# Kernel optimization log

Hardware: AMD Instinct MI355X
Metric: run time of the kernel (lower is better)

## Reference

```python
import jax, jax.numpy as jnp
import numpy as np

LOC_SIZE, CID_SIZE, UID_SIZE, TIM_SIZE = 10000, 300, 1000, 48
LOC_EMB, CID_EMB, UID_EMB, TIM_EMB = 256, 64, 64, 32
HID, ENC_HID = 500, 250            # hidden_size, history_hidden_size
SEQ, TGT = 2048, 256
INPUT = LOC_EMB + TIM_EMB + CID_EMB  # 352


def setup_inputs() -> dict:
    key = jax.random.key(0)
    ks = jax.random.split(key, 32)
    n = lambda i, shape, s=0.05: (jax.random.normal(ks[i], shape, dtype=jnp.float32) * s)
    d = {}
    d["loc"] = jax.random.randint(ks[0], (SEQ, 1), 0, LOC_SIZE)
    d["tim"] = jax.random.randint(ks[1], (SEQ, 1), 0, TIM_SIZE)
    d["cid"] = jax.random.randint(ks[2], (SEQ, 1), 0, CID_SIZE)
    d["uid"] = jax.random.randint(ks[3], (1,), 0, UID_SIZE)
    d["target"] = jax.random.randint(ks[4], (TGT, 1), 0, LOC_SIZE)
    d["target_len"] = TGT
    d["time_sim_matrix"] = jax.random.uniform(ks[5], (TIM_SIZE, TIM_SIZE), dtype=jnp.float32)
    # keep distances away from 0 since the model computes 1/dist
    d["poi_distance_matrix"] = jax.random.uniform(ks[6], (LOC_SIZE, LOC_SIZE), dtype=jnp.float32, minval=0.1, maxval=2.0)
    d["poi_cid_tim"] = jax.random.uniform(ks[7], (TIM_SIZE, CID_SIZE), dtype=jnp.float32)
    # embedding tables (emb_loc/emb_cid are pretrained+frozen in the original)
    d["weight"] = n(8, (LOC_SIZE, LOC_EMB))
    d["weight_cid"] = n(9, (CID_SIZE, CID_EMB))
    d["emb_uid_w"] = n(10, (UID_SIZE, UID_EMB))
    d["emb_tim_w"] = n(11, (TIM_SIZE, TIM_EMB))
    # bidirectional encoder LSTM (hidden 250), gate order i,f,g,o like torch
    d["enc_Wih_f"] = n(12, (4 * ENC_HID, INPUT))
    d["enc_Whh_f"] = n(13, (4 * ENC_HID, ENC_HID))
    d["enc_b_f"] = jnp.zeros((4 * ENC_HID,), jnp.float32)
    d["enc_Wih_b"] = n(14, (4 * ENC_HID, INPUT))
    d["enc_Whh_b"] = n(15, (4 * ENC_HID, ENC_HID))
    d["enc_b_b"] = jnp.zeros((4 * ENC_HID,), jnp.float32)
    # decoder LSTM (hidden 500)
    d["dec_Wih"] = n(16, (4 * HID, INPUT))
    d["dec_Whh"] = n(17, (4 * HID, HID))
    d["dec_b"] = jnp.zeros((4 * HID,), jnp.float32)
    # linear layers
    d["fc_user_w"] = n(18, (HID, UID_EMB))
    d["fc_user_b"] = jnp.zeros((HID,), jnp.float32)
    d["fc_final_w"] = n(19, (LOC_SIZE, 3 * HID))
    d["fc_final_b"] = jnp.zeros((LOC_SIZE,), jnp.float32)
    d["fc_final2_w"] = n(20, (HID, 3 * HID))
    d["fc_final2_b"] = jnp.zeros((HID,), jnp.float32)
    return d


def _lstm(x, Wih, Whh, b, H):
    """Single-layer LSTM, batch=1. x: [T, D] -> hs: [T, H]."""
    h0 = jnp.zeros((H,), x.dtype)
    c0 = jnp.zeros((H,), x.dtype)

    def step(carry, xt):
        h, c = carry
        z = Wih @ xt + Whh @ h + b
        i, f, g, o = jnp.split(z, 4)
        c = jax.nn.sigmoid(f) * c + jax.nn.sigmoid(i) * jnp.tanh(g)
        h = jax.nn.sigmoid(o) * jnp.tanh(c)
        return (h, c), h

    _, hs = jax.lax.scan(step, (h0, c0), x)
    return hs


def _table_attn(history, current, table, invert=False, causal=False):
    """Vectorized replacement for the nested-loop lookup attention.
    energies[i, j] = table[current[i], history[j]] (or its reciprocal),
    upper triangle left at 0 for the self-attn variants (as in the original),
    then softmax over the full row (torch F.softmax default dim=1 on 2D)."""
    e = table[current[:, None], history[None, :]]
    if invert:
        e = 1.0 / e
    if causal:
        nn_ = e.shape[0]
        e = jnp.where(jnp.tril(jnp.ones((nn_, nn_), bool)), e, jnp.zeros((), e.dtype))
    return jax.nn.softmax(e, axis=-1)


def reference(loc, tim, cid, uid, target, target_len,
              time_sim_matrix, poi_distance_matrix, poi_cid_tim,
              weight, weight_cid, emb_uid_w, emb_tim_w,
              enc_Wih_f, enc_Whh_f, enc_b_f, enc_Wih_b, enc_Whh_b, enc_b_b,
              dec_Wih, dec_Whh, dec_b,
              fc_user_w, fc_user_b, fc_final_w, fc_final_b, fc_final2_w, fc_final2_b):
    T = int(target_len)
    loc_f, tim_f, cid_f = loc[:, 0], tim[:, 0], cid[:, 0]

    # cross attention: current window attends to history via lookup tables
    attn_cid_time = _table_attn(cid_f[:-T], tim_f[-T:], poi_cid_tim)
    attn_loc = _table_attn(loc_f[:-T], loc_f[-T:], poi_distance_matrix, invert=True)
    attn_time = _table_attn(tim_f[:-T], tim_f[-T:], time_sim_matrix)
    # self attention on the current window (lower-triangular fill)
    self_cid_time = _table_attn(cid_f[-T:], tim_f[-T:], poi_cid_tim, causal=True)
    self_loc = _table_attn(loc_f[-T:], loc_f[-T:], poi_distance_matrix, invert=True, causal=True)
    self_time = _table_attn(tim_f[-T:], tim_f[-T:], time_sim_matrix, causal=True)

    # embeddings (dropout is identity in eval)
    x = jnp.concatenate([weight[loc_f], emb_tim_w[tim_f], weight_cid[cid_f]], axis=1)  # [SEQ, INPUT]
    hist_x, tgt_x = x[:-T], x[-T:]

    # bidirectional encoder over history
    hf = _lstm(hist_x, enc_Wih_f, enc_Whh_f, enc_b_f, ENC_HID)
    hb = _lstm(hist_x[::-1], enc_Wih_b, enc_Whh_b, enc_b_b, ENC_HID)[::-1]
    hidden_history = jnp.concatenate([hf, hb], axis=1)  # [SEQ-T, 2*ENC_HID=500]

    # decoder over current window
    hidden_state = _lstm(tgt_x, dec_Wih, dec_Whh, dec_b, HID)  # [T, 500]

    target_emb = weight[target[:, 0]]  # [T, LOC_EMB]

    uid_emb = emb_uid_w[uid] @ fc_user_w.T + fc_user_b  # [1, 500]
    user_attn = jax.nn.softmax(uid_emb @ hidden_history.T, axis=-1)  # [1, hist]
    context_user = user_attn @ hidden_history  # [1, 500]

    context = (attn_loc + attn_time + attn_cid_time) @ hidden_history  # [T, 500]
    hidden_state = (self_loc + self_time + self_cid_time) @ hidden_state  # [T, 500]

    hidden_state_all = hidden_state + uid_emb  # broadcast of repeat
    out = jnp.concatenate([hidden_state_all, context,
                           jnp.broadcast_to(context_user, (T, HID))], axis=1)  # [T, 1500]
    y = out @ fc_final_w.T + fc_final_b    # [T, LOC_SIZE]
    y1 = out @ fc_final2_w.T + fc_final2_b  # [T, HID]
    score = jax.nn.log_softmax(y, axis=-1)
    return score, y1, target_emb
```

## Files before the change

### kernel.cpp

```cpp
#include <hip/hip_runtime.h>
#include <stdint.h>

#define HIST 1792
#define TGT 256
#define SEQ 2048
#define INPUT 352
#define EHID 250
#define HID 500

typedef _Float16 h2_t __attribute__((ext_vector_type(2)));

static __device__ __forceinline__ float fdot2(uint32_t a, uint32_t b, float c) {
  return __builtin_amdgcn_fdot2(__builtin_bit_cast(h2_t, a),
                                __builtin_bit_cast(h2_t, b), c, false);
}
static __device__ __forceinline__ uint32_t packh2(float lo, float hi) {
  h2_t h; h[0] = (_Float16)lo; h[1] = (_Float16)hi;
  return __builtin_bit_cast(uint32_t, h);
}
static __device__ __forceinline__ uint4 packq(const float* p) {
  uint4 r;
  r.x = packh2(p[0], p[1]); r.y = packh2(p[2], p[3]);
  r.z = packh2(p[4], p[5]); r.w = packh2(p[6], p[7]);
  return r;
}
static __device__ __forceinline__ float dotq(uint4 w, uint4 h, float acc) {
  acc = fdot2(w.x, h.x, acc); acc = fdot2(w.y, h.y, acc);
  acc = fdot2(w.z, h.z, acc); acc = fdot2(w.w, h.w, acc);
  return acc;
}
static __device__ __forceinline__ float sigf(float x) {
  x = fminf(fmaxf(x, -30.f), 30.f);
  return 1.f / (1.f + __expf(-x));
}
static __device__ __forceinline__ float tanh_f(float x) {
  x = fminf(fmaxf(x, -15.f), 15.f);
  float e = __expf(2.f * x);
  return (e - 1.f) / (e + 1.f);
}
static __device__ __forceinline__ void spin_flag(volatile int* f) {
  while (__hip_atomic_load(f, __ATOMIC_ACQUIRE, __HIP_MEMORY_SCOPE_AGENT) == 0)
    __builtin_amdgcn_s_sleep(2);
}
#define AW(dst, src) asm("v_accvgpr_write_b32 %0, %1" : "=a"(dst) : "v"(src))
#define AR(dst, src) asm("v_accvgpr_read_b32 %0, %1" : "=v"(dst) : "a"(src))
#define ARQ(dst, arr, base) do { AR(dst.x, arr[(base)+0]); AR(dst.y, arr[(base)+1]); AR(dst.z, arr[(base)+2]); AR(dst.w, arr[(base)+3]); } while(0)

__global__ void k_embed(const int* __restrict__ loc, const int* __restrict__ tim,
                        const int* __restrict__ cid, const int* __restrict__ target,
                        const float* __restrict__ weight, const float* __restrict__ emb_tim_w,
                        const float* __restrict__ weight_cid,
                        float* __restrict__ x, float* __restrict__ te) {
  int t = blockIdx.x, tid = threadIdx.x;
  if (t < SEQ) {
    int l = loc[t], tm = tim[t], cd = cid[t];
    float* xr = x + (size_t)t * INPUT;
    for (int k = tid; k < 256; k += blockDim.x) xr[k] = weight[(size_t)l * 256 + k];
    for (int k = tid; k < 32; k += blockDim.x)  xr[256 + k] = emb_tim_w[tm * 32 + k];
    for (int k = tid; k < 64; k += blockDim.x)  xr[288 + k] = weight_cid[cd * 64 + k];
  } else {
    int i = t - SEQ;
    int tg = target[i];
    for (int k = tid; k < 256; k += blockDim.x) te[(size_t)i * 256 + k] = weight[(size_t)tg * 256 + k];
  }
}

__global__ void k_gemm_t16(const float* __restrict__ A, int lda,
                           const float* __restrict__ W, const float* __restrict__ bias,
                           float* __restrict__ C, int ldc,
                           int M, int N, int K, int revA) {
  __shared__ uint32_t AsP[8][65];
  __shared__ uint32_t WsP[8][65];
  const int bn = blockIdx.x * 64, bm = blockIdx.y * 64;
  const int tid = threadIdx.x;
  const int tx = tid & 15, ty = tid >> 4;
  float acc[4][4] = {};
  for (int k0 = 0; k0 < K; k0 += 16) {
    for (int i = tid; i < 512; i += 256) {
      int m = i & 63, kk = i >> 6;
      int gm = bm + m, gk = k0 + 2 * kk;
      float v0 = 0.f, v1 = 0.f;
      if (gm < M) {
        int am = revA ? (M - 1 - gm) : gm;
        if (gk < K)     v0 = A[(size_t)am * lda + gk];
        if (gk + 1 < K) v1 = A[(size_t)am * lda + gk + 1];
      }
      AsP[kk][m] = packh2(v0, v1);
    }
    for (int i = tid; i < 512; i += 256) {
      int n = i & 63, kk = i >> 6;
      int gn = bn + n, gk = k0 + 2 * kk;
      float v0 = 0.f, v1 = 0.f;
      if (gn < N) {
        if (gk < K)     v0 = W[(size_t)gn * K + gk];
        if (gk + 1 < K) v1 = W[(size_t)gn * K + gk + 1];
      }
      WsP[kk][n] = packh2(v0, v1);
    }
    __syncthreads();
#pragma unroll
    for (int kk = 0; kk < 8; kk++) {
      uint32_t a0 = AsP[kk][ty * 4 + 0], a1 = AsP[kk][ty * 4 + 1], a2 = AsP[kk][ty * 4 + 2], a3 = AsP[kk][ty * 4 + 3];
      uint32_t b0 = WsP[kk][tx * 4 + 0], b1 = WsP[kk][tx * 4 + 1], b2 = WsP[kk][tx * 4 + 2], b3 = WsP[kk][tx * 4 + 3];
      acc[0][0] = fdot2(a0, b0, acc[0][0]); acc[0][1] = fdot2(a0, b1, acc[0][1]);
      acc[0][2] = fdot2(a0, b2, acc[0][2]); acc[0][3] = fdot2(a0, b3, acc[0][3]);
      acc[1][0] = fdot2(a1, b0, acc[1][0]); acc[1][1] = fdot2(a1, b1, acc[1][1]);
      acc[1][2] = fdot2(a1, b2, acc[1][2]); acc[1][3] = fdot2(a1, b3, acc[1][3]);
      acc[2][0] = fdot2(a2, b0, acc[2][0]); acc[2][1] = fdot2(a2, b1, acc[2][1]);
      acc[2][2] = fdot2(a2, b2, acc[2][2]); acc[2][3] = fdot2(a2, b3, acc[2][3]);
      acc[3][0] = fdot2(a3, b0, acc[3][0]); acc[3][1] = fdot2(a3, b1, acc[3][1]);
      acc[3][2] = fdot2(a3, b2, acc[3][2]); acc[3][3] = fdot2(a3, b3, acc[3][3]);
    }
    __syncthreads();
  }
  for (int i = 0; i < 4; i++) {
    int gm = bm + ty * 4 + i; if (gm >= M) continue;
    for (int j = 0; j < 4; j++) {
      int gn = bn + tx * 4 + j; if (gn >= N) continue;
      C[(size_t)gm * ldc + gn] = acc[i][j] + (bias ? bias[gn] : 0.f);
    }
  }
}

__global__ void k_gemm_nn16(const float* __restrict__ A, int lda,
                            const float* __restrict__ B, int ldb,
                            const float* __restrict__ addvec,
                            float* __restrict__ C, int ldc,
                            int M, int N, int K) {
  __shared__ uint32_t AsP[8][65];
  __shared__ uint32_t BsP[8][65];
  const int bn = blockIdx.x * 64, bm = blockIdx.y * 64;
  const int tid = threadIdx.x;
  const int tx = tid & 15, ty = tid >> 4;
  float acc[4][4] = {};
  for (int k0 = 0; k0 < K; k0 += 16) {
    for (int i = tid; i < 512; i += 256) {
      int m = i & 63, kk = i >> 6;
      int gm = bm + m, gk = k0 + 2 * kk;
      float v0 = 0.f, v1 = 0.f;
      if (gm < M) {
        if (gk < K)     v0 = A[(size_t)gm * lda + gk];
        if (gk + 1 < K) v1 = A[(size_t)gm * lda + gk + 1];
      }
      AsP[kk][m] = packh2(v0, v1);
    }
    for (int i = tid; i < 512; i += 256) {
      int n = i & 63, kk = i >> 6;
      int gn = bn + n, gk = k0 + 2 * kk;
      float v0 = 0.f, v1 = 0.f;
      if (gn < N) {
        if (gk < K)     v0 = B[(size_t)gk * ldb + gn];
        if (gk + 1 < K) v1 = B[(size_t)(gk + 1) * ldb + gn];
      }
      BsP[kk][n] = packh2(v0, v1);
    }
    __syncthreads();
#pragma unroll
    for (int kk = 0; kk < 8; kk++) {
      uint32_t a0 = AsP[kk][ty * 4 + 0], a1 = AsP[kk][ty * 4 + 1], a2 = AsP[kk][ty * 4 + 2], a3 = AsP[kk][ty * 4 + 3];
      uint32_t b0 = BsP[kk][tx * 4 + 0], b1 = BsP[kk][tx * 4 + 1], b2 = BsP[kk][tx * 4 + 2], b3 = BsP[kk][tx * 4 + 3];
      acc[0][0] = fdot2(a0, b0, acc[0][0]); acc[0][1] = fdot2(a0, b1, acc[0][1]);
      acc[0][2] = fdot2(a0, b2, acc[0][2]); acc[0][3] = fdot2(a0, b3, acc[0][3]);
      acc[1][0] = fdot2(a1, b0, acc[1][0]); acc[1][1] = fdot2(a1, b1, acc[1][1]);
      acc[1][2] = fdot2(a1, b2, acc[1][2]); acc[1][3] = fdot2(a1, b3, acc[1][3]);
      acc[2][0] = fdot2(a2, b0, acc[2][0]); acc[2][1] = fdot2(a2, b1, acc[2][1]);
      acc[2][2] = fdot2(a2, b2, acc[2][2]); acc[2][3] = fdot2(a2, b3, acc[2][3]);
      acc[3][0] = fdot2(a3, b0, acc[3][0]); acc[3][1] = fdot2(a3, b1, acc[3][1]);
      acc[3][2] = fdot2(a3, b2, acc[3][2]); acc[3][3] = fdot2(a3, b3, acc[3][3]);
    }
    __syncthreads();
  }
  for (int i = 0; i < 4; i++) {
    int gm = bm + ty * 4 + i; if (gm >= M) continue;
    for (int j = 0; j < 4; j++) {
      int gn = bn + tx * 4 + j; if (gn >= N) continue;
      C[(size_t)gm * ldc + gn] = acc[i][j] + (addvec ? addvec[gn] : 0.f);
    }
  }
}

#define WQL 12
#define WBYTES (WQL * 512 * 16)
__launch_bounds__(512)
__global__ void k_lstm(const float* __restrict__ A_f, const float* __restrict__ A_b,
                       const float* __restrict__ A_d,
                       const float* __restrict__ Whh_f, const float* __restrict__ Whh_b,
                       const float* __restrict__ Whh_d,
                       float* __restrict__ hh, float* __restrict__ hdec,
                       float* zpub, uint32_t* hpub, int* flag_z, int* flag_h) {
  const int b = blockIdx.x;
  const int tid = threadIdx.x;
  __shared__ __align__(16) unsigned char smem[WBYTES + 2048];
  uint4* wl = (uint4*)smem;
  uint4* hbuf = (uint4*)(smem + WBYTES);

  if (tid < 128) hbuf[tid] = make_uint4(0, 0, 0, 0);

  if (b < 2) {
    const float* A = (b == 0) ? A_f : A_b;
    const float* Whh = (b == 0) ? Whh_f : Whh_b;
    const bool act = tid < 500;
    const int cell = act ? (tid >> 1) : 249;
    const int role = tid & 1;
    const int row0 = role * 250 + cell;
    const int row1 = 500 + role * 250 + cell;
    uint4 wv0[10], wv1[10];
    uint32_t wa[128];
    if (act) {
      const float* wr0 = Whh + (size_t)row0 * EHID;
      const float* wr1 = Whh + (size_t)row1 * EHID;
#pragma unroll
      for (int q = 0; q < 6; q++) {
        float t0[8], t1[8];
#pragma unroll
        for (int cc = 0; cc < 8; cc++) {
          int col = 208 + 8 * q + cc;
          t0[cc] = (col < EHID) ? wr0[col] : 0.f;
          t1[cc] = (col < EHID) ? wr1[col] : 0.f;
        }
        wl[(q * 2 + 0) * 512 + tid] = packq(t0);
        wl[(q * 2 + 1) * 512 + tid] = packq(t1);
      }
#pragma unroll
      for (int k = 0; k < 16; k++) {
        uint4 p0 = packq(wr0 + 8 * (10 + k));
        uint4 p1 = packq(wr1 + 8 * (10 + k));
        AW(wa[k * 4 + 0], p0.x); AW(wa[k * 4 + 1], p0.y);
        AW(wa[k * 4 + 2], p0.z); AW(wa[k * 4 + 3], p0.w);
        AW(wa[64 + k * 4 + 0], p1.x); AW(wa[64 + k * 4 + 1], p1.y);
        AW(wa[64 + k * 4 + 2], p1.z); AW(wa[64 + k * 4 + 3], p1.w);
      }
#pragma unroll
      for (int q = 0; q < 10; q++) { wv0[q] = packq(wr0 + 8 * q); wv1[q] = packq(wr1 + 8 * q); }
    }
    float c = 0.f;
    float aA = act ? A[row0] : 0.f;
    float aB = act ? A[row1] : 0.f;
    __syncthreads();
    for (int t = 0; t < HIST; t++) {
      const uint4* hb = hbuf + (t & 1) * 32;
      float z_r0 = 0.f, z_r1 = 0.f;
      if (act) {
        float z0 = aA, z1 = aB, y0 = 0.f, y1 = 0.f;
        int tn = (t + 1 < HIST) ? t + 1 : t;
        aA = A[tn * 1000 + row0];
        aB = A[tn * 1000 + row1];
#pragma unroll
        for (int q = 0; q < 10; q++) {
          uint4 hq = hb[q];
          z0 = dotq(wv0[q], hq, z0);
          z1 = dotq(wv1[q], hq, z1);
        }
#pragma unroll
        for (int k = 0; k < 16; k++) {
          uint4 hq = hb[10 + k];
          uint4 u0, u1;
          ARQ(u0, wa, k * 4);
          ARQ(u1, wa, 64 + k * 4);
          y0 = dotq(u0, hq, y0);
          y1 = dotq(u1, hq, y1);
        }
#pragma unroll
        for (int q = 0; q < 6; q++) {
          uint4 hq = hb[26 + q];
          z0 = dotq(wl[(q * 2 + 0) * 512 + tid], hq, z0);
          z1 = dotq(wl[(q * 2 + 1) * 512 + tid], hq, z1);
        }
        z_r0 = z0 + y0;
        z_r1 = z1 + y1;
      }
      float pA = __shfl_xor(z_r0, 1);
      float pB = __shfl_xor(z_r1, 1);
      float zi = role ? pA : z_r0;
      float zf = role ? z_r0 : pA;
      float zg = role ? pB : z_r1;
      float zo = role ? z_r1 : pB;
      float hval = 0.f;
      if (act) {
        c = sigf(zf) * c + sigf(zi) * tanh_f(zg);
        hval = sigf(zo) * tanh_f(c);
        if (role == 0) {
          if (b == 0) hh[(size_t)t * HID + cell] = hval;
          else        hh[(size_t)(HIST - 1 - t) * HID + EHID + cell] = hval;
        }
      }
      float hn = __shfl_xor(hval, 2);
      uint32_t* hw = (uint32_t*)(hbuf + ((t + 1) & 1) * 32);
      if (act && (tid & 3) == 0) hw[tid >> 2] = packh2(hval, hn);
      __syncthreads();
    }
  } else {
    const int gi = b - 2;
    const int j = tid;
    const bool act = (j < 500);
    uint4 wv[20];
    uint32_t wa[128];
    if (act) {
      const float* wr = Whh_d + (size_t)(gi * 500 + j) * HID;
#pragma unroll
      for (int q = 0; q < 12; q++) {
        float tmp[8];
#pragma unroll
        for (int cc = 0; cc < 8; cc++) {
          int col = 416 + 8 * q + cc;
          tmp[cc] = (col < HID) ? wr[col] : 0.f;
        }
        wl[q * 512 + tid] = packq(tmp);
      }
#pragma unroll
      for (int k = 0; k < 32; k++) {
        uint4 pq = packq(wr + 8 * (20 + k));
        AW(wa[k * 4 + 0], pq.x); AW(wa[k * 4 + 1], pq.y);
        AW(wa[k * 4 + 2], pq.z); AW(wa[k * 4 + 3], pq.w);
      }
#pragma unroll
      for (int q = 0; q < 20; q++) wv[q] = packq(wr + 8 * q);
    }
    float c = 0.f;
    float aD = act ? A_d[gi * 500 + j] : 0.f;
    __syncthreads();
    for (int t = 0; t < TGT; t++) {
      const uint4* hb = hbuf + (t & 1) * 64;
      float z = 0.f;
      if (act) {
        float z0 = aD, z1 = 0.f, z2 = 0.f, z3 = 0.f;
        int tn = (t + 1 < TGT) ? t + 1 : t;
        aD = A_d[tn * 2000 + gi * 500 + j];
#pragma unroll
        for (int q = 0; q < 20; q += 2) {
          z0 = dotq(wv[q], hb[q], z0);
          z1 = dotq(wv[q + 1], hb[q + 1], z1);
        }
#pragma unroll
        for (int k = 0; k < 32; k += 2) {
          uint4 u0, u1;
          ARQ(u0, wa, k * 4);
          ARQ(u1, wa, (k + 1) * 4);
          z2 = dotq(u0, hb[20 + k], z2);
          z3 = dotq(u1, hb[21 + k], z3);
        }
#pragma unroll
        for (int q = 0; q < 12; q += 2) {
          z0 = dotq(wl[q * 512 + tid], hb[52 + q], z0);
          z1 = dotq(wl[(q + 1) * 512 + tid], hb[53 + q], z1);
        }
        z = (z0 + z1) + (z2 + z3);
      }
      if (gi < 3) {
        if (act) zpub[gi * 512 + j] = z;
        __threadfence();
        __syncthreads();
        if (tid == 0) {
          __hip_atomic_store(&flag_z[t * 3 + gi], 1, __ATOMIC_RELEASE, __HIP_MEMORY_SCOPE_AGENT);
          spin_flag(&flag_h[t]);
        }
        __syncthreads();
        uint32_t* hw = (uint32_t*)(hbuf + ((t + 1) & 1) * 64);
        if (tid < 250)
          hw[tid] = __hip_atomic_load(&hpub[tid], __ATOMIC_RELAXED, __HIP_MEMORY_SCOPE_AGENT);
        __syncthreads();
      } else {
        if (tid == 0) {
          spin_flag(&flag_z[t * 3 + 0]);
          spin_flag(&flag_z[t * 3 + 1]);
          spin_flag(&flag_z[t * 3 + 2]);
        }
        __syncthreads();
        float hval = 0.f;
        if (act) {
          float zi = __hip_atomic_load(&zpub[0 * 512 + j], __ATOMIC_RELAXED, __HIP_MEMORY_SCOPE_AGENT);
          float zf = __hip_atomic_load(&zpub[1 * 512 + j], __ATOMIC_RELAXED, __HIP_MEMORY_SCOPE_AGENT);
          float zg = __hip_atomic_load(&zpub[2 * 512 + j], __ATOMIC_RELAXED, __HIP_MEMORY_SCOPE_AGENT);
          c = sigf(zf) * c + sigf(zi) * tanh_f(zg);
          hval = sigf(z) * tanh_f(c);
          hdec[(size_t)t * HID + j] = hval;
        }
        float hother = __shfl_xor(hval, 1);
        uint32_t* hw = (uint32_t*)(hbuf + ((t + 1) & 1) * 64);
        if (act && !(j & 1)) {
          uint32_t p = packh2(hval, hother);
          hw[j >> 1] = p;
          __hip_atomic_store(&hpub[j >> 1], p, __ATOMIC_RELAXED, __HIP_MEMORY_SCOPE_AGENT);
        }
        __threadfence();
        __syncthreads();
        if (tid == 0)
          __hip_atomic_store(&flag_h[t], 1, __ATOMIC_RELEASE, __HIP_MEMORY_SCOPE_AGENT);
      }
    }
  }
}

__global__ void k_attn(const int* __restrict__ loc, const int* __restrict__ tim,
                       const int* __restrict__ cid,
                       const float* __restrict__ ts, const float* __restrict__ pd,
                       const float* __restrict__ pct,
                       float* __restrict__ S1, float* __restrict__ S2) {
  const int i = blockIdx.x;
  const int tid = threadIdx.x;
  __shared__ float e[HIST];
  __shared__ float red[256];
  const int loc_i = loc[HIST + i], tim_i = tim[HIST + i];
  for (int tab = 0; tab < 3; tab++) {
    for (int jj = tid; jj < HIST; jj += 256) {
      float v;
      if (tab == 0)      v = 1.f / pd[(size_t)loc_i * 10000 + loc[jj]];
      else if (tab == 1) v = ts[tim_i * 48 + tim[jj]];
      else               v = pct[tim_i * 300 + cid[jj]];
      e[jj] = v;
    }
    __syncthreads();
    float mx = -1e30f;
    for (int jj = tid; jj < HIST; jj += 256) mx = fmaxf(mx, e[jj]);
    red[tid] = mx; __syncthreads();
    for (int s = 128; s > 0; s >>= 1) { if (tid < s) red[tid] = fmaxf(red[tid], red[tid + s]); __syncthreads(); }
    mx = red[0]; __syncthreads();
    float sm = 0.f;
    for (int jj = tid; jj < HIST; jj += 256) sm += __expf(e[jj] - mx);
    red[tid] = sm; __syncthreads();
    for (int s = 128; s > 0; s >>= 1) { if (tid < s) red[tid] += red[tid + s]; __syncthreads(); }
    float inv = 1.f / red[0]; __syncthreads();
    for (int jj = tid; jj < HIST; jj += 256) {
      float p = __expf(e[jj] - mx) * inv;
      if (tab == 0) S1[(size_t)i * HIST + jj] = p; else S1[(size_t)i * HIST + jj] += p;
    }
    __syncthreads();
  }
  const int lj = loc[HIST + tid], tj = tim[HIST + tid], cj = cid[HIST + tid];
  for (int tab = 0; tab < 3; tab++) {
    float v;
    if (tab == 0)      v = 1.f / pd[(size_t)loc_i * 10000 + lj];
    else if (tab == 1) v = ts[tim_i * 48 + tj];
    else               v = pct[tim_i * 300 + cj];
    if (tid > i) v = 0.f;
    red[tid] = v; __syncthreads();
    for (int s = 128; s > 0; s >>= 1) { if (tid < s) red[tid] = fmaxf(red[tid], red[tid + s]); __syncthreads(); }
    float mx = red[0]; __syncthreads();
    float ex = __expf(v - mx);
    red[tid] = ex; __syncthreads();
    for (int s = 128; s > 0; s >>= 1) { if (tid < s) red[tid] += red[tid + s]; __syncthreads(); }
    float p = ex / red[0]; __syncthreads();
    if (tab == 0) S2[(size_t)i * TGT + tid] = p; else S2[(size_t)i * TGT + tid] += p;
    __syncthreads();
  }
}

__global__ void k_uid(const int* __restrict__ uid, const float* __restrict__ emb_uid_w,
                      const float* __restrict__ fc_user_w, const float* __restrict__ fc_user_b,
                      float* __restrict__ uid_emb) {
  const int tid = threadIdx.x;
  __shared__ float u[64];
  if (tid < 64) u[tid] = emb_uid_w[(size_t)uid[0] * 64 + tid];
  __syncthreads();
  if (tid < HID) {
    float a = fc_user_b[tid];
    for (int k = 0; k < 64; k++) a += u[k] * fc_user_w[tid * 64 + k];
    uid_emb[tid] = a;
  }
}

__global__ void k_user(const float* __restrict__ uid_emb, const float* __restrict__ hh,
                       float* __restrict__ out) {
  const int tid = threadIdx.x;
  __shared__ float s[HIST];
  __shared__ float red[1024];
  __shared__ float ue[HID];
  if (tid < HID) ue[tid] = uid_emb[tid];
  __syncthreads();
  for (int t = tid; t < HIST; t += 1024) {
    float a = 0.f;
    const float* hr = hh + (size_t)t * HID;
    for (int k = 0; k < HID; k++) a += ue[k] * hr[k];
    s[t] = a;
  }
  __syncthreads();
  float mx = -1e30f;
  for (int t = tid; t < HIST; t += 1024) mx = fmaxf(mx, s[t]);
  red[tid] = mx; __syncthreads();
  for (int st = 512; st > 0; st >>= 1) { if (tid < st) red[tid] = fmaxf(red[tid], red[tid + st]); __syncthreads(); }
  mx = red[0]; __syncthreads();
  float sm = 0.f;
  for (int t = tid; t < HIST; t += 1024) sm += __expf(s[t] - mx);
  red[tid] = sm; __syncthreads();
  for (int st = 512; st > 0; st >>= 1) { if (tid < st) red[tid] += red[tid + st]; __syncthreads(); }
  float inv = 1.f / red[0]; __syncthreads();
  for (int t = tid; t < HIST; t += 1024) s[t] = __expf(s[t] - mx) * inv;
  __syncthreads();
  if (tid < HID) {
    float a = 0.f;
    for (int t = 0; t < HIST; t++) a += s[t] * hh[(size_t)t * HID + tid];
    for (int i = 0; i < TGT; i++) out[(size_t)i * 1500 + 1000 + tid] = a;
  }
}

__global__ void k_logsoftmax(float* __restrict__ y) {
  const int i = blockIdx.x;
  const int tid = threadIdx.x;
  float* r = y + (size_t)i * 10000;
  __shared__ float red[1024];
  float mx = -1e30f;
  for (int j = tid; j < 10000; j += 1024) mx = fmaxf(mx, r[j]);
  red[tid] = mx; __syncthreads();
  for (int s = 512; s > 0; s >>= 1) { if (tid < s) red[tid] = fmaxf(red[tid], red[tid + s]); __syncthreads(); }
  mx = red[0]; __syncthreads();
  float sm = 0.f;
  for (int j = tid; j < 10000; j += 1024) sm += __expf(r[j] - mx);
  red[tid] = sm; __syncthreads();
  for (int s = 512; s > 0; s >>= 1) { if (tid < s) red[tid] += red[tid + s]; __syncthreads(); }
  float lse = mx + __logf(red[0]);
  __syncthreads();
  for (int j = tid; j < 10000; j += 1024) r[j] = r[j] - lse;
}

extern "C" void kernel_launch(void* const* d_in, const int* in_sizes, int n_in,
                              void* d_out, int out_size, void* d_ws, size_t ws_size,
                              hipStream_t stream) {
  (void)in_sizes; (void)n_in; (void)out_size; (void)ws_size;
  const int* loc = (const int*)d_in[0];
  const int* tim = (const int*)d_in[1];
  const int* cid = (const int*)d_in[2];
  const int* uid = (const int*)d_in[3];
  const int* target = (const int*)d_in[4];
  const float* ts = (const float*)d_in[6];
  const float* pd = (const float*)d_in[7];
  const float* pct = (const float*)d_in[8];
  const float* weight = (const float*)d_in[9];
  const float* weight_cid = (const float*)d_in[10];
  const float* emb_uid_w = (const float*)d_in[11];
  const float* emb_tim_w = (const float*)d_in[12];
  const float* enc_Wih_f = (const float*)d_in[13];
  const float* enc_Whh_f = (const float*)d_in[14];
  const float* enc_b_f = (const float*)d_in[15];
  const float* enc_Wih_b = (const float*)d_in[16];
  const float* enc_Whh_b = (const float*)d_in[17];
  const float* enc_b_b = (const float*)d_in[18];
  const float* dec_Wih = (const float*)d_in[19];
  const float* dec_Whh = (const float*)d_in[20];
  const float* dec_b = (const float*)d_in[21];
  const float* fc_user_w = (const float*)d_in[22];
  const float* fc_user_b = (const float*)d_in[23];
  const float* fc_final_w = (const float*)d_in[24];
  const float* fc_final_b = (const float*)d_in[25];
  const float* fc_final2_w = (const float*)d_in[26];
  const float* fc_final2_b = (const float*)d_in[27];

  float* score = (float*)d_out;
  float* y1 = score + (size_t)TGT * 10000;
  float* te = y1 + (size_t)TGT * HID;

  float* ws = (float*)d_ws;
  float* x = ws;
  float* A_f = x + (size_t)SEQ * INPUT;
  float* A_b = A_f + (size_t)HIST * 1000;
  float* A_d = A_b + (size_t)HIST * 1000;
  float* hh = A_d + (size_t)TGT * 2000;
  float* hdec = hh + (size_t)HIST * HID;
  float* S1 = hdec + (size_t)TGT * HID;
  float* S2 = S1 + (size_t)TGT * HIST;
  float* outb = S2 + (size_t)TGT * TGT;
  float* uid_emb = outb + (size_t)TGT * 1500;
  float* zpub = uid_emb + 512;
  uint32_t* hpub = (uint32_t*)(zpub + 3 * 512);
  int* flag_z = (int*)(hpub + 256);
  int* flag_h = flag_z + 3 * TGT;

  k_embed<<<dim3(SEQ + TGT), dim3(128), 0, stream>>>(loc, tim, cid, target, weight, emb_tim_w, weight_cid, x, te);

  k_gemm_t16<<<dim3(16, 28), dim3(256), 0, stream>>>(x, INPUT, enc_Wih_f, enc_b_f, A_f, 1000, HIST, 1000, INPUT, 0);
  k_gemm_t16<<<dim3(16, 28), dim3(256), 0, stream>>>(x, INPUT, enc_Wih_b, enc_b_b, A_b, 1000, HIST, 1000, INPUT, 1);
  k_gemm_t16<<<dim3(32, 4), dim3(256), 0, stream>>>(x + (size_t)HIST * INPUT, INPUT, dec_Wih, dec_b, A_d, 2000, TGT, 2000, INPUT, 0);

  hipMemsetAsync(flag_z, 0, 4 * TGT * sizeof(int), stream);

  k_attn<<<dim3(TGT), dim3(256), 0, stream>>>(loc, tim, cid, ts, pd, pct, S1, S2);
  k_uid<<<dim3(1), dim3(512), 0, stream>>>(uid, emb_uid_w, fc_user_w, fc_user_b, uid_emb);

  k_lstm<<<dim3(6), dim3(512), 0, stream>>>(A_f, A_b, A_d, enc_Whh_f, enc_Whh_b, dec_Whh,
                                            hh, hdec, zpub, hpub, flag_z, flag_h);

  k_user<<<dim3(1), dim3(1024), 0, stream>>>(uid_emb, hh, outb);
  k_gemm_nn16<<<dim3(8, 4), dim3(256), 0, stream>>>(S2, TGT, hdec, HID, uid_emb, outb, 1500, TGT, HID, TGT);
  k_gemm_nn16<<<dim3(8, 4), dim3(256), 0, stream>>>(S1, HIST, hh, HID, nullptr, outb + 500, 1500, TGT, HID, HIST);

  k_gemm_t16<<<dim3(157, 4), dim3(256), 0, stream>>>(outb, 1500, fc_final_w, fc_final_b, score, 10000, TGT, 10000, 1500, 0);
  k_gemm_t16<<<dim3(8, 4), dim3(256), 0, stream>>>(outb, 1500, fc_final2_w, fc_final2_b, y1, 500, TGT, 500, 1500, 0);

  k_logsoftmax<<<dim3(TGT), dim3(1024), 0, stream>>>(score);
}
```

Baseline: 5.433 ms.

## Split encoder LSTM cells across K-halves instead of gate pairs per thread

Result: slower. 5.768 ms (+6.2%).

```diff
diff --git a/kernel.cpp b/kernel.cpp
--- a/kernel.cpp
+++ b/kernel.cpp
@@ -199,94 +199,86 @@
   if (b < 2) {
     const float* A = (b == 0) ? A_f : A_b;
     const float* Whh = (b == 0) ? Whh_f : Whh_b;
-    const bool act = tid < 500;
-    const int cell = act ? (tid >> 1) : 249;
-    const int role = tid & 1;
-    const int row0 = role * 250 + cell;
-    const int row1 = 500 + role * 250 + cell;
-    uint4 wv0[10], wv1[10];
+    const int r = (tid >> 6) * 32 + (tid & 31);
+    const int kh = (tid >> 5) & 1;
+    const bool act = r < 250;
+    const int colbase = kh * 128;
+    uint4 wv[20];
     uint32_t wa[128];
     if (act) {
-      const float* wr0 = Whh + (size_t)row0 * EHID;
-      const float* wr1 = Whh + (size_t)row1 * EHID;
-#pragma unroll
-      for (int q = 0; q < 6; q++) {
-        float t0[8], t1[8];
-#pragma unroll
-        for (int cc = 0; cc < 8; cc++) {
-          int col = 208 + 8 * q + cc;
-          t0[cc] = (col < EHID) ? wr0[col] : 0.f;
-          t1[cc] = (col < EHID) ? wr1[col] : 0.f;
-        }
-        wl[(q * 2 + 0) * 512 + tid] = packq(t0);
-        wl[(q * 2 + 1) * 512 + tid] = packq(t1);
-      }
-#pragma unroll
-      for (int k = 0; k < 16; k++) {
-        uint4 p0 = packq(wr0 + 8 * (10 + k));
-        uint4 p1 = packq(wr1 + 8 * (10 + k));
-        AW(wa[k * 4 + 0], p0.x); AW(wa[k * 4 + 1], p0.y);
-        AW(wa[k * 4 + 2], p0.z); AW(wa[k * 4 + 3], p0.w);
-        AW(wa[64 + k * 4 + 0], p1.x); AW(wa[64 + k * 4 + 1], p1.y);
-        AW(wa[64 + k * 4 + 2], p1.z); AW(wa[64 + k * 4 + 3], p1.w);
-      }
-#pragma unroll
-      for (int q = 0; q < 10; q++) { wv0[q] = packq(wr0 + 8 * q); wv1[q] = packq(wr1 + 8 * q); }
+#pragma unroll
+      for (int g = 0; g < 4; g++) {
+        const float* wr = Whh + (size_t)(g * 250 + r) * EHID + colbase;
+#pragma unroll
+        for (int q = 0; q < 16; q++) {
+          float tmp[8];
+#pragma unroll
+          for (int cc = 0; cc < 8; cc++) {
+            int col = colbase + 8 * q + cc;
+            tmp[cc] = (col < EHID) ? wr[8 * q + cc] : 0.f;
+          }
+          uint4 pq = packq(tmp);
+          const int wq = g * 16 + q;
+          if (wq < 20) wv[wq] = pq;
+          else if (wq < 52) {
+            AW(wa[(wq - 20) * 4 + 0], pq.x); AW(wa[(wq - 20) * 4 + 1], pq.y);
+            AW(wa[(wq - 20) * 4 + 2], pq.z); AW(wa[(wq - 20) * 4 + 3], pq.w);
+          } else wl[(wq - 52) * 512 + tid] = pq;
+        }
+      }
     }
     float c = 0.f;
-    float aA = act ? A[row0] : 0.f;
-    float aB = act ? A[row1] : 0.f;
+    float aN0 = 0.f, aN1 = 0.f, aN2 = 0.f, aN3 = 0.f;
+    if (kh == 0 && act) {
+      aN0 = A[r]; aN1 = A[250 + r]; aN2 = A[500 + r]; aN3 = A[750 + r];
+    }
     __syncthreads();
     for (int t = 0; t < HIST; t++) {
-      const uint4* hb = hbuf + (t & 1) * 32;
-      float z_r0 = 0.f, z_r1 = 0.f;
-      if (act) {
-        float z0 = aA, z1 = aB, y0 = 0.f, y1 = 0.f;
+      const uint4* hb = hbuf + (t & 1) * 32 + kh * 16;
+      float z0 = 0.f, z1 = 0.f, z2 = 0.f, z3 = 0.f;
+      float aC0 = aN0, aC1 = aN1, aC2 = aN2, aC3 = aN3;
+      if (kh == 0 && act) {
         int tn = (t + 1 < HIST) ? t + 1 : t;
-        aA = A[tn * 1000 + row0];
-        aB = A[tn * 1000 + row1];
-#pragma unroll
-        for (int q = 0; q < 10; q++) {
-          uint4 hq = hb[q];
-          z0 = dotq(wv0[q], hq, z0);
-          z1 = dotq(wv1[q], hq, z1);
-        }
-#pragma unroll
-        for (int k = 0; k < 16; k++) {
-          uint4 hq = hb[10 + k];
-          uint4 u0, u1;
-          ARQ(u0, wa, k * 4);
-          ARQ(u1, wa, 64 + k * 4);
-          y0 = dotq(u0, hq, y0);
-          y1 = dotq(u1, hq, y1);
-        }
-#pragma unroll
-        for (int q = 0; q < 6; q++) {
-          uint4 hq = hb[26 + q];
-          z0 = dotq(wl[(q * 2 + 0) * 512 + tid], hq, z0);
-          z1 = dotq(wl[(q * 2 + 1) * 512 + tid], hq, z1);
-        }
-        z_r0 = z0 + y0;
-        z_r1 = z1 + y1;
-      }
-      float pA = __shfl_xor(z_r0, 1);
-      float pB = __shfl_xor(z_r1, 1);
-      float zi = role ? pA : z_r0;
-      float zf = role ? z_r0 : pA;
-      float zg = role ? pB : z_r1;
-      float zo = role ? z_r1 : pB;
+        aN0 = A[tn * 1000 + r];       aN1 = A[tn * 1000 + 250 + r];
+        aN2 = A[tn * 1000 + 500 + r]; aN3 = A[tn * 1000 + 750 + r];
+      }
+#pragma unroll
+      for (int q = 0; q < 4; q++) {
+        uint4 hq = hb[q];
+        z0 = dotq(wv[q], hq, z0);
+        z1 = dotq(wv[16 + q], hq, z1);
+        uint4 u2; ARQ(u2, wa, (12 + q) * 4);
+        z2 = dotq(u2, hq, z2);
+        uint4 u3; ARQ(u3, wa, (28 + q) * 4);
+        z3 = dotq(u3, hq, z3);
+      }
+#pragma unroll
+      for (int q = 4; q < 16; q++) {
+        uint4 hq = hb[q];
+        z0 = dotq(wv[q], hq, z0);
+        uint4 u1; ARQ(u1, wa, (q - 4) * 4);
+        z1 = dotq(u1, hq, z1);
+        uint4 u2; ARQ(u2, wa, (12 + q) * 4);
+        z2 = dotq(u2, hq, z2);
+        z3 = dotq(wl[(q - 4) * 512 + tid], hq, z3);
+      }
+      if (kh == 0) { z0 += aC0; z1 += aC1; z2 += aC2; z3 += aC3; }
+      z0 += __shfl_xor(z0, 32);
+      z1 += __shfl_xor(z1, 32);
+      z2 += __shfl_xor(z2, 32);
+      z3 += __shfl_xor(z3, 32);
       float hval = 0.f;
       if (act) {
-        c = sigf(zf) * c + sigf(zi) * tanh_f(zg);
-        hval = sigf(zo) * tanh_f(c);
-        if (role == 0) {
-          if (b == 0) hh[(size_t)t * HID + cell] = hval;
-          else        hh[(size_t)(HIST - 1 - t) * HID + EHID + cell] = hval;
-        }
-      }
-      float hn = __shfl_xor(hval, 2);
+        c = sigf(z1) * c + sigf(z0) * tanh_f(z2);
+        hval = sigf(z3) * tanh_f(c);
+        if (kh == 0) {
+          if (b == 0) hh[(size_t)t * HID + r] = hval;
+          else        hh[(size_t)(HIST - 1 - t) * HID + EHID + r] = hval;
+        }
+      }
+      float hn = __shfl_xor(hval, 1);
       uint32_t* hw = (uint32_t*)(hbuf + ((t + 1) & 1) * 32);
-      if (act && (tid & 3) == 0) hw[tid >> 2] = packh2(hval, hn);
+      if (act && kh == 0 && !(r & 1)) hw[r >> 1] = packh2(hval, hn);
       __syncthreads();
     }
   } else {
```

## Fuse attention and uid kernels into LSTM launch; restructure encoder gate exchange via LDS

Applied to the files above, without the earlier changes.

Result: faster. 5.322 ms (-2.1%).

```diff
diff --git a/kernel.cpp b/kernel.cpp
--- a/kernel.cpp
+++ b/kernel.cpp
@@ -187,28 +187,33 @@
                        const float* __restrict__ Whh_f, const float* __restrict__ Whh_b,
                        const float* __restrict__ Whh_d,
                        float* __restrict__ hh, float* __restrict__ hdec,
-                       float* zpub, uint32_t* hpub, int* flag_z, int* flag_h) {
+                       float* zpub, uint32_t* hpub, int* flag_z, int* flag_h,
+                       const int* __restrict__ loc, const int* __restrict__ tim,
+                       const int* __restrict__ cid,
+                       const float* __restrict__ ts, const float* __restrict__ pd,
+                       const float* __restrict__ pct,
+                       float* __restrict__ S1, float* __restrict__ S2,
+                       const int* __restrict__ uid, const float* __restrict__ emb_uid_w,
+                       const float* __restrict__ fc_user_w, const float* __restrict__ fc_user_b,
+                       float* __restrict__ uid_emb) {
   const int b = blockIdx.x;
   const int tid = threadIdx.x;
-  __shared__ __align__(16) unsigned char smem[WBYTES + 2048];
+  __shared__ __align__(16) unsigned char smem[WBYTES + 2048 + 4096];
   uint4* wl = (uint4*)smem;
   uint4* hbuf = (uint4*)(smem + WBYTES);
-
-  if (tid < 128) hbuf[tid] = make_uint4(0, 0, 0, 0);
+  float* zbuf = (float*)(smem + WBYTES + 2048);
+
+  if (b < 6 && tid < 128) hbuf[tid] = make_uint4(0, 0, 0, 0);
 
   if (b < 2) {
     const float* A = (b == 0) ? A_f : A_b;
     const float* Whh = (b == 0) ? Whh_f : Whh_b;
     const bool act = tid < 500;
-    const int cell = act ? (tid >> 1) : 249;
-    const int role = tid & 1;
-    const int row0 = role * 250 + cell;
-    const int row1 = 500 + role * 250 + cell;
     uint4 wv0[10], wv1[10];
     uint32_t wa[128];
     if (act) {
-      const float* wr0 = Whh + (size_t)row0 * EHID;
-      const float* wr1 = Whh + (size_t)row1 * EHID;
+      const float* wr0 = Whh + (size_t)tid * EHID;
+      const float* wr1 = Whh + (size_t)(tid + 500) * EHID;
 #pragma unroll
       for (int q = 0; q < 6; q++) {
         float t0[8], t1[8];
@@ -234,17 +239,16 @@
       for (int q = 0; q < 10; q++) { wv0[q] = packq(wr0 + 8 * q); wv1[q] = packq(wr1 + 8 * q); }
     }
     float c = 0.f;
-    float aA = act ? A[row0] : 0.f;
-    float aB = act ? A[row1] : 0.f;
+    float aA = act ? A[tid] : 0.f;
+    float aB = act ? A[500 + tid] : 0.f;
     __syncthreads();
     for (int t = 0; t < HIST; t++) {
       const uint4* hb = hbuf + (t & 1) * 32;
-      float z_r0 = 0.f, z_r1 = 0.f;
       if (act) {
         float z0 = aA, z1 = aB, y0 = 0.f, y1 = 0.f;
         int tn = (t + 1 < HIST) ? t + 1 : t;
-        aA = A[tn * 1000 + row0];
-        aB = A[tn * 1000 + row1];
+        aA = A[tn * 1000 + tid];
+        aB = A[tn * 1000 + 500 + tid];
 #pragma unroll
         for (int q = 0; q < 10; q++) {
           uint4 hq = hb[q];
@@ -266,30 +270,24 @@
           z0 = dotq(wl[(q * 2 + 0) * 512 + tid], hq, z0);
           z1 = dotq(wl[(q * 2 + 1) * 512 + tid], hq, z1);
         }
-        z_r0 = z0 + y0;
-        z_r1 = z1 + y1;
-      }
-      float pA = __shfl_xor(z_r0, 1);
-      float pB = __shfl_xor(z_r1, 1);
-      float zi = role ? pA : z_r0;
-      float zf = role ? z_r0 : pA;
-      float zg = role ? pB : z_r1;
-      float zo = role ? z_r1 : pB;
+        zbuf[tid] = z0 + y0;
+        zbuf[500 + tid] = z1 + y1;
+      }
+      __syncthreads();
       float hval = 0.f;
-      if (act) {
+      if (tid < EHID) {
+        float zi = zbuf[tid], zf = zbuf[250 + tid], zg = zbuf[500 + tid], zo = zbuf[750 + tid];
         c = sigf(zf) * c + sigf(zi) * tanh_f(zg);
         hval = sigf(zo) * tanh_f(c);
-        if (role == 0) {
-          if (b == 0) hh[(size_t)t * HID + cell] = hval;
-          else        hh[(size_t)(HIST - 1 - t) * HID + EHID + cell] = hval;
-        }
-      }
-      float hn = __shfl_xor(hval, 2);
+        if (b == 0) hh[(size_t)t * HID + tid] = hval;
+        else        hh[(size_t)(HIST - 1 - t) * HID + EHID + tid] = hval;
+      }
+      float hother = __shfl_xor(hval, 1);
       uint32_t* hw = (uint32_t*)(hbuf + ((t + 1) & 1) * 32);
-      if (act && (tid & 3) == 0) hw[tid >> 2] = packh2(hval, hn);
-      __syncthreads();
-    }
-  } else {
+      if (tid < EHID && !(tid & 1)) hw[tid >> 1] = packh2(hval, hother);
+      __syncthreads();
+    }
+  } else if (b < 6) {
     const int gi = b - 2;
     const int j = tid;
     const bool act = (j < 500);
@@ -388,74 +386,69 @@
           __hip_atomic_store(&flag_h[t], 1, __ATOMIC_RELEASE, __HIP_MEMORY_SCOPE_AGENT);
       }
     }
-  }
-}
-
-__global__ void k_attn(const int* __restrict__ loc, const int* __restrict__ tim,
-                       const int* __restrict__ cid,
-                       const float* __restrict__ ts, const float* __restrict__ pd,
-                       const float* __restrict__ pct,
-                       float* __restrict__ S1, float* __restrict__ S2) {
-  const int i = blockIdx.x;
-  const int tid = threadIdx.x;
-  __shared__ float e[HIST];
-  __shared__ float red[256];
-  const int loc_i = loc[HIST + i], tim_i = tim[HIST + i];
-  for (int tab = 0; tab < 3; tab++) {
-    for (int jj = tid; jj < HIST; jj += 256) {
-      float v;
-      if (tab == 0)      v = 1.f / pd[(size_t)loc_i * 10000 + loc[jj]];
-      else if (tab == 1) v = ts[tim_i * 48 + tim[jj]];
-      else               v = pct[tim_i * 300 + cid[jj]];
-      e[jj] = v;
-    }
-    __syncthreads();
-    float mx = -1e30f;
-    for (int jj = tid; jj < HIST; jj += 256) mx = fmaxf(mx, e[jj]);
-    red[tid] = mx; __syncthreads();
-    for (int s = 128; s > 0; s >>= 1) { if (tid < s) red[tid] = fmaxf(red[tid], red[tid + s]); __syncthreads(); }
-    mx = red[0]; __syncthreads();
-    float sm = 0.f;
-    for (int jj = tid; jj < HIST; jj += 256) sm += __expf(e[jj] - mx);
-    red[tid] = sm; __syncthreads();
-    for (int s = 128; s > 0; s >>= 1) { if (tid < s) red[tid] += red[tid + s]; __syncthreads(); }
-    float inv = 1.f / red[0]; __syncthreads();
-    for (int jj = tid; jj < HIST; jj += 256) {
-      float p = __expf(e[jj] - mx) * inv;
-      if (tab == 0) S1[(size_t)i * HIST + jj] = p; else S1[(size_t)i * HIST + jj] += p;
-    }
-    __syncthreads();
-  }
-  const int lj = loc[HIST + tid], tj = tim[HIST + tid], cj = cid[HIST + tid];
-  for (int tab = 0; tab < 3; tab++) {
-    float v;
-    if (tab == 0)      v = 1.f / pd[(size_t)loc_i * 10000 + lj];
-    else if (tab == 1) v = ts[tim_i * 48 + tj];
-    else               v = pct[tim_i * 300 + cj];
-    if (tid > i) v = 0.f;
-    red[tid] = v; __syncthreads();
-    for (int s = 128; s > 0; s >>= 1) { if (tid < s) red[tid] = fmaxf(red[tid], red[tid + s]); __syncthreads(); }
-    float mx = red[0]; __syncthreads();
-    float ex = __expf(v - mx);
-    red[tid] = ex; __syncthreads();
-    for (int s = 128; s > 0; s >>= 1) { if (tid < s) red[tid] += red[tid + s]; __syncthreads(); }
-    float p = ex / red[0]; __syncthreads();
-    if (tab == 0) S2[(size_t)i * TGT + tid] = p; else S2[(size_t)i * TGT + tid] += p;
-    __syncthreads();
-  }
-}
-
-__global__ void k_uid(const int* __restrict__ uid, const float* __restrict__ emb_uid_w,
-                      const float* __restrict__ fc_user_w, const float* __restrict__ fc_user_b,
-                      float* __restrict__ uid_emb) {
-  const int tid = threadIdx.x;
-  __shared__ float u[64];
-  if (tid < 64) u[tid] = emb_uid_w[(size_t)uid[0] * 64 + tid];
-  __syncthreads();
-  if (tid < HID) {
-    float a = fc_user_b[tid];
-    for (int k = 0; k < 64; k++) a += u[k] * fc_user_w[tid * 64 + k];
-    uid_emb[tid] = a;
+  } else if (b < 262) {
+    const int i = b - 6;
+    float* e = (float*)smem;
+    float* red = ((float*)smem) + HIST;
+    const int loc_i = loc[HIST + i], tim_i = tim[HIST + i];
+    for (int tab = 0; tab < 3; tab++) {
+      for (int jj = tid; jj < HIST; jj += 512) {
+        float v;
+        if (tab == 0)      v = 1.f / pd[(size_t)loc_i * 10000 + loc[jj]];
+        else if (tab == 1) v = ts[tim_i * 48 + tim[jj]];
+        else               v = pct[tim_i * 300 + cid[jj]];
+        e[jj] = v;
+      }
+      __syncthreads();
+      float mx = -1e30f;
+      for (int jj = tid; jj < HIST; jj += 512) mx = fmaxf(mx, e[jj]);
+      red[tid] = mx; __syncthreads();
+      for (int s = 256; s > 0; s >>= 1) { if (tid < s) red[tid] = fmaxf(red[tid], red[tid + s]); __syncthreads(); }
+      mx = red[0]; __syncthreads();
+      float sm = 0.f;
+      for (int jj = tid; jj < HIST; jj += 512) sm += __expf(e[jj] - mx);
+      red[tid] = sm; __syncthreads();
+      for (int s = 256; s > 0; s >>= 1) { if (tid < s) red[tid] += red[tid + s]; __syncthreads(); }
+      float inv = 1.f / red[0]; __syncthreads();
+      for (int jj = tid; jj < HIST; jj += 512) {
+        float p = __expf(e[jj] - mx) * inv;
+        if (tab == 0) S1[(size_t)i * HIST + jj] = p; else S1[(size_t)i * HIST + jj] += p;
+      }
+      __syncthreads();
+    }
+    int lj = 0, tj = 0, cj = 0;
+    if (tid < TGT) { lj = loc[HIST + tid]; tj = tim[HIST + tid]; cj = cid[HIST + tid]; }
+    for (int tab = 0; tab < 3; tab++) {
+      float v = 0.f;
+      if (tid < TGT) {
+        if (tab == 0)      v = 1.f / pd[(size_t)loc_i * 10000 + lj];
+        else if (tab == 1) v = ts[tim_i * 48 + tj];
+        else               v = pct[tim_i * 300 + cj];
+        if (tid > i) v = 0.f;
+        red[tid] = v;
+      }
+      __syncthreads();
+      for (int s = 128; s > 0; s >>= 1) { if (tid < s) red[tid] = fmaxf(red[tid], red[tid + s]); __syncthreads(); }
+      float mx = red[0]; __syncthreads();
+      float ex = (tid < TGT) ? __expf(v - mx) : 0.f;
+      if (tid < TGT) red[tid] = ex;
+      __syncthreads();
+      for (int s = 128; s > 0; s >>= 1) { if (tid < s) red[tid] += red[tid + s]; __syncthreads(); }
+      float p = ex / red[0]; __syncthreads();
+      if (tid < TGT) {
+        if (tab == 0) S2[(size_t)i * TGT + tid] = p; else S2[(size_t)i * TGT + tid] += p;
+      }
+      __syncthreads();
+    }
+  } else {
+    float* u = (float*)smem;
+    if (tid < 64) u[tid] = emb_uid_w[(size_t)uid[0] * 64 + tid];
+    __syncthreads();
+    if (tid < HID) {
+      float a = fc_user_b[tid];
+      for (int k = 0; k < 64; k++) a += u[k] * fc_user_w[tid * 64 + k];
+      uid_emb[tid] = a;
+    }
   }
 }
 
@@ -464,13 +457,18 @@
   const int tid = threadIdx.x;
   __shared__ float s[HIST];
   __shared__ float red[1024];
-  __shared__ float ue[HID];
+  __shared__ __align__(16) float ue[HID];
   if (tid < HID) ue[tid] = uid_emb[tid];
   __syncthreads();
   for (int t = tid; t < HIST; t += 1024) {
+    const float4* hr = (const float4*)(hh + (size_t)t * HID);
+    const float4* uv = (const float4*)ue;
     float a = 0.f;
-    const float* hr = hh + (size_t)t * HID;
-    for (int k = 0; k < HID; k++) a += ue[k] * hr[k];
+#pragma unroll 5
+    for (int k = 0; k < 125; k++) {
+      float4 h4 = hr[k], u4 = uv[k];
+      a += h4.x * u4.x + h4.y * u4.y + h4.z * u4.z + h4.w * u4.w;
+    }
     s[t] = a;
   }
   __syncthreads();
@@ -487,8 +485,14 @@
   for (int t = tid; t < HIST; t += 1024) s[t] = __expf(s[t] - mx) * inv;
   __syncthreads();
   if (tid < HID) {
-    float a = 0.f;
-    for (int t = 0; t < HIST; t++) a += s[t] * hh[(size_t)t * HID + tid];
+    float a0 = 0.f, a1 = 0.f, a2 = 0.f, a3 = 0.f;
+    for (int t = 0; t < HIST; t += 4) {
+      a0 += s[t]     * hh[(size_t)t * HID + tid];
+      a1 += s[t + 1] * hh[(size_t)(t + 1) * HID + tid];
+      a2 += s[t + 2] * hh[(size_t)(t + 2) * HID + tid];
+      a3 += s[t + 3] * hh[(size_t)(t + 3) * HID + tid];
+    }
+    float a = (a0 + a1) + (a2 + a3);
     for (int i = 0; i < TGT; i++) out[(size_t)i * 1500 + 1000 + tid] = a;
   }
 }
@@ -572,11 +576,10 @@
 
   hipMemsetAsync(flag_z, 0, 4 * TGT * sizeof(int), stream);
 
-  k_attn<<<dim3(TGT), dim3(256), 0, stream>>>(loc, tim, cid, ts, pd, pct, S1, S2);
-  k_uid<<<dim3(1), dim3(512), 0, stream>>>(uid, emb_uid_w, fc_user_w, fc_user_b, uid_emb);
-
-  k_lstm<<<dim3(6), dim3(512), 0, stream>>>(A_f, A_b, A_d, enc_Whh_f, enc_Whh_b, dec_Whh,
-                                            hh, hdec, zpub, hpub, flag_z, flag_h);
+  k_lstm<<<dim3(263), dim3(512), 0, stream>>>(A_f, A_b, A_d, enc_Whh_f, enc_Whh_b, dec_Whh,
+                                              hh, hdec, zpub, hpub, flag_z, flag_h,
+                                              loc, tim, cid, ts, pd, pct, S1, S2,
+                                              uid, emb_uid_w, fc_user_w, fc_user_b, uid_emb);
 
   k_user<<<dim3(1), dim3(1024), 0, stream>>>(uid_emb, hh, outb);
   k_gemm_nn16<<<dim3(8, 4), dim3(256), 0, stream>>>(S2, TGT, hdec, HID, uid_emb, outb, 1500, TGT, HID, TGT);
```
